# Kernel tuning notes

Hardware: AMD Instinct MI355X
Metric: run time of the kernel (lower is better)

## Reference

```python
import jax, jax.numpy as jnp
import numpy as np
import math

B, H, T, DH, D = 1, 8, 2048, 64, 64
NEG_INF = -1e30
EPS = 1e-9

def setup_inputs() -> dict:
    key = jax.random.key(0)
    ks = jax.random.split(key, 6)
    q = jax.random.normal(ks[0], (B, H, T, DH), dtype=jnp.float32)
    k = jax.random.normal(ks[1], (B, H, T, DH), dtype=jnp.float32)
    v = jax.random.normal(ks[2], (B, H, T, DH), dtype=jnp.float32)
    edge_type_bias = 0.1 * jax.random.normal(ks[3], (4,), dtype=jnp.float32)
    neigh_idx = jax.random.randint(ks[4], (H, T, D), 0, T).astype(jnp.int32)
    edge_type = jax.random.randint(ks[5], (H, T, D), 0, 5).astype(jnp.int32)
    return {"q": q, "k": k, "v": v, "edge_type_bias": edge_type_bias,
            "neigh_idx": neigh_idx, "edge_type": edge_type}

def _masked_softmax(scores, mask):
    # scores: [B,H,T,D] fp32, mask: [1,H,T,D] bool; zeros on all-masked rows
    masked = jnp.where(mask, scores, NEG_INF)
    m = jnp.max(masked, axis=-1, keepdims=True)
    e = jnp.where(mask, jnp.exp(masked - m), 0.0)
    denom = jnp.maximum(jnp.sum(e, axis=-1, keepdims=True), EPS)
    return e / denom

def reference(q, k, v, edge_type_bias, neigh_idx, edge_type):
    Bq, Hq, Tq, dh = q.shape
    # safe_neighbor_idx: clamp to valid range
    s_idx = jnp.clip(neigh_idx, 0, Tq - 1)                       # [H,T,D]
    # causal_neighbor_mask: valid (>=0) and neighbor <= query position
    pos = jnp.arange(Tq, dtype=neigh_idx.dtype)[None, :, None]    # [1,T,1]
    mask = (neigh_idx >= 0) & (neigh_idx <= pos)                  # [H,T,D]
    # edge-type bias: type 0 -> no bias, types 1..4 -> learnable bias
    full_bias = jnp.concatenate([jnp.zeros((1,), jnp.float32),
                                 edge_type_bias.astype(jnp.float32)])
    bias_htd = full_bias[edge_type]                               # [H,T,D]
    # gather neighbor K/V: k_g[b,h,t,n,:] = k[b,h,s_idx[h,t,n],:]
    h_ix = jnp.arange(Hq)[:, None, None]                          # [H,1,1]
    k_g = k[:, h_ix, s_idx]                                       # [B,H,T,D,dh]
    v_g = v[:, h_ix, s_idx]                                       # [B,H,T,D,dh]
    scores = jnp.einsum('bhtc,bhtnc->bhtn',
                        q.astype(jnp.float32),
                        k_g.astype(jnp.float32)) / math.sqrt(dh)
    scores = scores + bias_htd[None]                              # [B,H,T,D]
    w = _masked_softmax(scores, mask[None])                       # [B,H,T,D]
    y = jnp.einsum('bhtn,bhtnc->bhtc', w, v_g.astype(jnp.float32))
    return y.astype(v.dtype)
```

## Files before the change

### kernel.cpp

```cpp
#include <hip/hip_runtime.h>
#include <hip/hip_fp16.h>

constexpr int H  = 8;
constexpr int T  = 2048;
constexpr int DH = 64;
constexpr int D  = 64;
constexpr int NKV = H * T * DH;

typedef _Float16 half2v __attribute__((ext_vector_type(2)));

#if defined(__has_builtin)
#if __has_builtin(__builtin_amdgcn_fdot2)
#define HAVE_FDOT2 1
#endif
#if __has_builtin(__builtin_amdgcn_permlane32_swap)
#define HAVE_PL32 1
#endif
#if __has_builtin(__builtin_amdgcn_permlane16_swap)
#define HAVE_PL16 1
#endif
#endif

__device__ __forceinline__ float dot2acc(half2v a, half2v b, float c) {
#ifdef HAVE_FDOT2
    return __builtin_amdgcn_fdot2(a, b, c, false);
#else
    return c + (float)a.x * (float)b.x + (float)a.y * (float)b.y;
#endif
}

__device__ __forceinline__ half2v h2bits(int b) { return __builtin_bit_cast(half2v, b); }

__device__ __forceinline__ half2v f2h2(float x, float y) {
    __half2 h = __float22half2_rn(make_float2(x, y));
    return __builtin_bit_cast(half2v, h);
}

__device__ __forceinline__ float xor32add_f(float x) {
#ifdef HAVE_PL32
    unsigned u = __builtin_bit_cast(unsigned, x);
    auto r = __builtin_amdgcn_permlane32_swap(u, u, false, false);
    return __builtin_bit_cast(float, (unsigned)r[0]) + __builtin_bit_cast(float, (unsigned)r[1]);
#else
    return x + __shfl_xor(x, 32);
#endif
}
__device__ __forceinline__ float xor32max_f(float x) {
#ifdef HAVE_PL32
    unsigned u = __builtin_bit_cast(unsigned, x);
    auto r = __builtin_amdgcn_permlane32_swap(u, u, false, false);
    return fmaxf(__builtin_bit_cast(float, (unsigned)r[0]), __builtin_bit_cast(float, (unsigned)r[1]));
#else
    return fmaxf(x, __shfl_xor(x, 32));
#endif
}
__device__ __forceinline__ float xor16add_f(float x) {
#ifdef HAVE_PL16
    unsigned u = __builtin_bit_cast(unsigned, x);
    auto r = __builtin_amdgcn_permlane16_swap(u, u, false, false);
    return __builtin_bit_cast(float, (unsigned)r[0]) + __builtin_bit_cast(float, (unsigned)r[1]);
#else
    return x + __shfl_xor(x, 16);
#endif
}
__device__ __forceinline__ float xor16max_f(float x) {
#ifdef HAVE_PL16
    unsigned u = __builtin_bit_cast(unsigned, x);
    auto r = __builtin_amdgcn_permlane16_swap(u, u, false, false);
    return fmaxf(__builtin_bit_cast(float, (unsigned)r[0]), __builtin_bit_cast(float, (unsigned)r[1]));
#else
    return fmaxf(x, __shfl_xor(x, 16));
#endif
}
__device__ __forceinline__ half2v xor32add_h2(half2v x) {
#ifdef HAVE_PL32
    unsigned u = __builtin_bit_cast(unsigned, x);
    auto r = __builtin_amdgcn_permlane32_swap(u, u, false, false);
    return h2bits((int)r[0]) + h2bits((int)r[1]);
#else
    return x + h2bits(__shfl_xor(__builtin_bit_cast(int, x), 32));
#endif
}
__device__ __forceinline__ half2v xor16add_h2(half2v x) {
#ifdef HAVE_PL16
    unsigned u = __builtin_bit_cast(unsigned, x);
    auto r = __builtin_amdgcn_permlane16_swap(u, u, false, false);
    return h2bits((int)r[0]) + h2bits((int)r[1]);
#else
    return x + h2bits(__shfl_xor(__builtin_bit_cast(int, x), 16));
#endif
}
__device__ __forceinline__ half2v xor8add_h2(half2v x) {
    return x + h2bits(__shfl_xor(__builtin_bit_cast(int, x), 8));
}

__global__ __launch_bounds__(256) void cvt_f32_f16(
    const float* __restrict__ k, const float* __restrict__ v,
    __half* __restrict__ kh, __half* __restrict__ vh)
{
    const int i = (blockIdx.x * 256 + threadIdx.x) * 8;
    const float* src = (blockIdx.y == 0) ? k : v;
    __half*      dst = (blockIdx.y == 0) ? kh : vh;
    const float4 a = *reinterpret_cast<const float4*>(src + i);
    const float4 b = *reinterpret_cast<const float4*>(src + i + 4);
    __half2 hh[4];
    hh[0] = __float22half2_rn(make_float2(a.x, a.y));
    hh[1] = __float22half2_rn(make_float2(a.z, a.w));
    hh[2] = __float22half2_rn(make_float2(b.x, b.y));
    hh[3] = __float22half2_rn(make_float2(b.z, b.w));
    *reinterpret_cast<float4*>(dst + i) = *reinterpret_cast<const float4*>(hh);
}

__global__ __launch_bounds__(256, 5) void wayfinder_attn_f16(
    const float* __restrict__ q,
    const __half* __restrict__ kh,
    const __half* __restrict__ vh,
    const float* __restrict__ eb,
    const int*   __restrict__ nidx,
    const int*   __restrict__ etyp,
    float* __restrict__ out)
{
    __shared__ __half vlds[4][8][512];

    const int wave = threadIdx.x >> 6;
    const int lane = threadIdx.x & 63;
    const int bid  = blockIdx.x;
    const int work = ((bid & 7) << 9) | (bid >> 3);
    const int flat = (work << 2) + wave;
    const int h    = flat >> 11;
    const int t    = flat & (T - 1);
    const int grp  = lane >> 3;
    const int sub  = lane & 7;

    const long long rowoff = (long long)flat * DH;
    const int*      nrow   = nidx + (long long)flat * D;
    const int*      erow   = etyp + (long long)flat * D;

    const int4 i0 = *reinterpret_cast<const int4*>(nrow + grp * 8);
    const int4 i1 = *reinterpret_cast<const int4*>(nrow + grp * 8 + 4);
    const int4 e0 = *reinterpret_cast<const int4*>(erow + grp * 8);
    const int4 e1 = *reinterpret_cast<const int4*>(erow + grp * 8 + 4);

    const float4 qa = *reinterpret_cast<const float4*>(q + rowoff + sub * 8);
    const float4 qb = *reinterpret_cast<const float4*>(q + rowoff + sub * 8 + 4);

    const int idx_i[8] = {i0.x, i0.y, i0.z, i0.w, i1.x, i1.y, i1.z, i1.w};
    const int et_i [8] = {e0.x, e0.y, e0.z, e0.w, e1.x, e1.y, e1.z, e1.w};

    const __half* khead = kh + (long long)h * T * DH;
    const __half* vhead = vh + (long long)h * T * DH;

    int s_i[8];
    int mskbits = 0;
    #pragma unroll
    for (int i = 0; i < 8; ++i) {
        s_i[i] = min(max(idx_i[i], 0), T - 1);
        mskbits |= ((idx_i[i] >= 0) && (idx_i[i] <= t)) ? (1 << i) : 0;
    }

    float4 kf[8];
    #pragma unroll
    for (int i = 0; i < 8; ++i)
        kf[i] = *reinterpret_cast<const float4*>(khead + (long long)s_i[i] * DH + sub * 8);

    #pragma unroll
    for (int i = 0; i < 8; ++i) {
        const __half* src = vhead + (long long)s_i[i] * DH + sub * 8;
        __builtin_amdgcn_global_load_lds(
            (const __attribute__((address_space(1))) void*)src,
            (__attribute__((address_space(3))) void*)(&vlds[wave][i][0]),
            16, 0, 0);
    }

    const float4 ebv = *reinterpret_cast<const float4*>(eb);
    float bias_i[8];
    #pragma unroll
    for (int i = 0; i < 8; ++i) {
        const int et = et_i[i];
        bias_i[i] = (et == 1) ? ebv.x : (et == 2) ? ebv.y :
                    (et == 3) ? ebv.z : (et == 4) ? ebv.w : 0.0f;
    }

    half2v qp[4];
    qp[0] = f2h2(qa.x, qa.y);
    qp[1] = f2h2(qa.z, qa.w);
    qp[2] = f2h2(qb.x, qb.y);
    qp[3] = f2h2(qb.z, qb.w);

    float sc[8];
    #pragma unroll
    for (int i = 0; i < 8; ++i) {
        const half2v* kp = reinterpret_cast<const half2v*>(&kf[i]);
        float p = dot2acc(qp[0], kp[0],
                  dot2acc(qp[1], kp[1],
                  dot2acc(qp[2], kp[2],
                  dot2acc(qp[3], kp[3], 0.0f))));
        p += __shfl_xor(p, 1);
        p += __shfl_xor(p, 2);
        p += __shfl_xor(p, 4);
        sc[i] = p;
    }

    float masked[8];
    float mx = -1e30f;
    #pragma unroll
    for (int i = 0; i < 8; ++i) {
        const bool mk = (mskbits >> i) & 1;
        masked[i] = mk ? fmaf(sc[i], 0.125f, bias_i[i]) : -1e30f;
        mx = fmaxf(mx, masked[i]);
    }
    mx = fmaxf(mx, __shfl_xor(mx, 8));
    mx = xor16max_f(mx);
    mx = xor32max_f(mx);

    float e[8];
    float sum = 0.0f;
    #pragma unroll
    for (int i = 0; i < 8; ++i) {
        const bool mk = (mskbits >> i) & 1;
        e[i] = mk ? __expf(masked[i] - mx) : 0.0f;
        sum += e[i];
    }
    sum += __shfl_xor(sum, 8);
    sum = xor16add_f(sum);
    sum = xor32add_f(sum);
    const float rden = 1.0f / fmaxf(sum, 1e-9f);

    asm volatile("s_waitcnt vmcnt(0)" ::: "memory");

    float acc[8] = {0.f, 0.f, 0.f, 0.f, 0.f, 0.f, 0.f, 0.f};
    #pragma unroll
    for (int i = 0; i < 8; ++i) {
        const float w = e[i] * rden;
        const float4 vfi = *reinterpret_cast<const float4*>(&vlds[wave][i][lane * 8]);
        const half2v* vp = reinterpret_cast<const half2v*>(&vfi);
        acc[0] += w * (float)vp[0].x;  acc[1] += w * (float)vp[0].y;
        acc[2] += w * (float)vp[1].x;  acc[3] += w * (float)vp[1].y;
        acc[4] += w * (float)vp[2].x;  acc[5] += w * (float)vp[2].y;
        acc[6] += w * (float)vp[3].x;  acc[7] += w * (float)vp[3].y;
    }

    half2v h0 = f2h2(acc[0], acc[1]);
    half2v h1 = f2h2(acc[2], acc[3]);
    half2v h2 = f2h2(acc[4], acc[5]);
    half2v h3 = f2h2(acc[6], acc[7]);
    h0 = xor8add_h2(h0);  h1 = xor8add_h2(h1);
    h2 = xor8add_h2(h2);  h3 = xor8add_h2(h3);
    h0 = xor16add_h2(h0); h1 = xor16add_h2(h1);
    h2 = xor16add_h2(h2); h3 = xor16add_h2(h3);
    h0 = xor32add_h2(h0); h1 = xor32add_h2(h1);
    h2 = xor32add_h2(h2); h3 = xor32add_h2(h3);

    if (lane < 16) {
        const int s8   = (lane & 7) * 8;
        const int half = lane >> 3;
        const float4 o = half
            ? make_float4((float)h2.x, (float)h2.y, (float)h3.x, (float)h3.y)
            : make_float4((float)h0.x, (float)h0.y, (float)h1.x, (float)h1.y);
        *reinterpret_cast<float4*>(out + rowoff + s8 + half * 4) = o;
    }
}

__global__ __launch_bounds__(256) void wayfinder_attn_f32(
    const float* __restrict__ q, const float* __restrict__ k,
    const float* __restrict__ v, const float* __restrict__ eb,
    const int* __restrict__ nidx, const int* __restrict__ etyp,
    float* __restrict__ out)
{
    const int wave = threadIdx.x >> 6;
    const int lane = threadIdx.x & 63;
    const int flat = (blockIdx.x << 2) + wave;
    const int h    = flat >> 11;
    const int t    = flat & (T - 1);
    const int grp  = lane >> 4;
    const int sub  = lane & 15;

    __shared__ int    sidx[4][64];
    __shared__ float  ssc [4][64];
    __shared__ float2 swv [4][64];

    const long long rowoff = (long long)flat * DH;
    const long long noff = (long long)flat * D + lane;
    const int  idx = nidx[noff];
    const int  et  = etyp[noff];
    const int  s   = min(max(idx, 0), T - 1);
    const bool msk = (idx >= 0) && (idx <= t);
    const float4 ebv  = *reinterpret_cast<const float4*>(eb);
    const float  bias = (et == 1) ? ebv.x : (et == 2) ? ebv.y :
                        (et == 3) ? ebv.z : (et == 4) ? ebv.w : 0.0f;
    sidx[wave][lane] = s;
    const float4 qf = *reinterpret_cast<const float4*>(q + rowoff + sub * 4);
    __syncthreads();

    const float* khead = k + (long long)h * T * DH;
    #pragma unroll
    for (int i = 0; i < 16; ++i) {
        const int n  = i * 4 + grp;
        const int sn = sidx[wave][n];
        const float4 kf = *reinterpret_cast<const float4*>(khead + sn * DH + sub * 4);
        float p = qf.x * kf.x + qf.y * kf.y + qf.z * kf.z + qf.w * kf.w;
        p += __shfl_xor(p, 1);
        p += __shfl_xor(p, 2);
        p += __shfl_xor(p, 4);
        p += __shfl_xor(p, 8);
        if (sub == 0) ssc[wave][n] = p;
    }
    __syncthreads();

    const float sc     = ssc[wave][lane];
    const float masked = msk ? (sc * 0.125f + bias) : -1e30f;
    float mx = masked;
    #pragma unroll
    for (int off = 32; off > 0; off >>= 1) mx = fmaxf(mx, __shfl_xor(mx, off));
    const float e = msk ? __expf(masked - mx) : 0.0f;
    float sum = e;
    #pragma unroll
    for (int off = 32; off > 0; off >>= 1) sum += __shfl_xor(sum, off);
    const float w = e / fmaxf(sum, 1e-9f);
    swv[wave][lane] = make_float2(w, __int_as_float(s));
    __syncthreads();

    const float* vhead = v + (long long)h * T * DH;
    float4 acc = make_float4(0.f, 0.f, 0.f, 0.f);
    #pragma unroll
    for (int i = 0; i < 16; ++i) {
        const int    n  = i * 4 + grp;
        const float2 ws = swv[wave][n];
        const int    sn = __float_as_int(ws.y);
        const float4 vf = *reinterpret_cast<const float4*>(vhead + sn * DH + sub * 4);
        acc.x += ws.x * vf.x; acc.y += ws.x * vf.y;
        acc.z += ws.x * vf.z; acc.w += ws.x * vf.w;
    }
    #pragma unroll
    for (int off = 16; off <= 32; off <<= 1) {
        acc.x += __shfl_xor(acc.x, off); acc.y += __shfl_xor(acc.y, off);
        acc.z += __shfl_xor(acc.z, off); acc.w += __shfl_xor(acc.w, off);
    }
    if (lane < 16)
        *reinterpret_cast<float4*>(out + rowoff + sub * 4) = acc;
}

extern "C" void kernel_launch(void* const* d_in, const int* in_sizes, int n_in,
                              void* d_out, int out_size, void* d_ws, size_t ws_size,
                              hipStream_t stream) {
    const float* q    = (const float*)d_in[0];
    const float* k    = (const float*)d_in[1];
    const float* v    = (const float*)d_in[2];
    const float* eb   = (const float*)d_in[3];
    const int*   nidx = (const int*)d_in[4];
    const int*   etyp = (const int*)d_in[5];
    float* out = (float*)d_out;

    const size_t need = (size_t)2 * NKV * sizeof(__half);
    if (ws_size >= need) {
        __half* kh = (__half*)d_ws;
        __half* vh = kh + NKV;
        dim3 cgrid(NKV / (256 * 8), 2);
        hipLaunchKernelGGL(cvt_f32_f16, cgrid, dim3(256), 0, stream, k, v, kh, vh);
        hipLaunchKernelGGL(wayfinder_attn_f16, dim3(H * T / 4), dim3(256), 0, stream,
                           q, kh, vh, eb, nidx, etyp, out);
    } else {
        hipLaunchKernelGGL(wayfinder_attn_f32, dim3(H * T / 4), dim3(256), 0, stream,
                           q, k, v, eb, nidx, etyp, out);
    }
}
```

Before: 29.55 us.

## Load gathered V rows into registers and use DPP for lane reductions

Gathered V rows are now loaded directly into registers next to the K loads, replacing the asynchronous global-to-LDS copy. This removes the shared-memory buffer and the explicit vmcnt wait. The xor-1/2/4/8 shuffle reductions become DPP quad-permute and row-mirror moves, which avoid the cross-lane shuffle path. The min-occupancy hint in launch_bounds is dropped, so the compiler can use more registers for the extra 8 float4 V values, which may reduce occupancy and latency hiding.

```diff
diff --git a/kernel.cpp b/kernel.cpp
--- a/kernel.cpp
+++ b/kernel.cpp
@@ -35,6 +35,17 @@
     __half2 h = __float22half2_rn(make_float2(x, y));
     return __builtin_bit_cast(half2v, h);
 }
+
+template<int CTRL>
+__device__ __forceinline__ float dpp_mov_f(float x) {
+    int yi = __builtin_amdgcn_update_dpp(0, __builtin_bit_cast(int, x),
+                                         CTRL, 0xF, 0xF, true);
+    return __builtin_bit_cast(float, yi);
+}
+template<int CTRL>
+__device__ __forceinline__ float dpp_add_f(float x) { return x + dpp_mov_f<CTRL>(x); }
+template<int CTRL>
+__device__ __forceinline__ float dpp_max_f(float x) { return fmaxf(x, dpp_mov_f<CTRL>(x)); }
 
 __device__ __forceinline__ float xor32add_f(float x) {
 #ifdef HAVE_PL32
@@ -111,7 +122,7 @@
     *reinterpret_cast<float4*>(dst + i) = *reinterpret_cast<const float4*>(hh);
 }
 
-__global__ __launch_bounds__(256, 5) void wayfinder_attn_f16(
+__global__ __launch_bounds__(256) void wayfinder_attn_f16(
     const float* __restrict__ q,
     const __half* __restrict__ kh,
     const __half* __restrict__ vh,
@@ -120,8 +131,6 @@
     const int*   __restrict__ etyp,
     float* __restrict__ out)
 {
-    __shared__ __half vlds[4][8][512];
-
     const int wave = threadIdx.x >> 6;
     const int lane = threadIdx.x & 63;
     const int bid  = blockIdx.x;
@@ -158,18 +167,12 @@
         mskbits |= ((idx_i[i] >= 0) && (idx_i[i] <= t)) ? (1 << i) : 0;
     }
 
-    float4 kf[8];
-    #pragma unroll
-    for (int i = 0; i < 8; ++i)
-        kf[i] = *reinterpret_cast<const float4*>(khead + (long long)s_i[i] * DH + sub * 8);
-
-    #pragma unroll
-    for (int i = 0; i < 8; ++i) {
-        const __half* src = vhead + (long long)s_i[i] * DH + sub * 8;
-        __builtin_amdgcn_global_load_lds(
-            (const __attribute__((address_space(1))) void*)src,
-            (__attribute__((address_space(3))) void*)(&vlds[wave][i][0]),
-            16, 0, 0);
+    float4 kf[8], vf[8];
+    #pragma unroll
+    for (int i = 0; i < 8; ++i) {
+        const long long ro = (long long)s_i[i] * DH + sub * 8;
+        kf[i] = *reinterpret_cast<const float4*>(khead + ro);
+        vf[i] = *reinterpret_cast<const float4*>(vhead + ro);
     }
 
     const float4 ebv = *reinterpret_cast<const float4*>(eb);
@@ -195,9 +198,9 @@
                   dot2acc(qp[1], kp[1],
                   dot2acc(qp[2], kp[2],
                   dot2acc(qp[3], kp[3], 0.0f))));
-        p += __shfl_xor(p, 1);
-        p += __shfl_xor(p, 2);
-        p += __shfl_xor(p, 4);
+        p = dpp_add_f<0xB1>(p);
+        p = dpp_add_f<0x4E>(p);
+        p = dpp_add_f<0x141>(p);
         sc[i] = p;
     }
 
@@ -209,7 +212,7 @@
         masked[i] = mk ? fmaf(sc[i], 0.125f, bias_i[i]) : -1e30f;
         mx = fmaxf(mx, masked[i]);
     }
-    mx = fmaxf(mx, __shfl_xor(mx, 8));
+    mx = dpp_max_f<0x140>(mx);
     mx = xor16max_f(mx);
     mx = xor32max_f(mx);
 
@@ -221,19 +224,16 @@
         e[i] = mk ? __expf(masked[i] - mx) : 0.0f;
         sum += e[i];
     }
-    sum += __shfl_xor(sum, 8);
+    sum = dpp_add_f<0x140>(sum);
     sum = xor16add_f(sum);
     sum = xor32add_f(sum);
     const float rden = 1.0f / fmaxf(sum, 1e-9f);
 
-    asm volatile("s_waitcnt vmcnt(0)" ::: "memory");
-
     float acc[8] = {0.f, 0.f, 0.f, 0.f, 0.f, 0.f, 0.f, 0.f};
     #pragma unroll
     for (int i = 0; i < 8; ++i) {
         const float w = e[i] * rden;
-        const float4 vfi = *reinterpret_cast<const float4*>(&vlds[wave][i][lane * 8]);
-        const half2v* vp = reinterpret_cast<const half2v*>(&vfi);
+        const half2v* vp = reinterpret_cast<const half2v*>(&vf[i]);
         acc[0] += w * (float)vp[0].x;  acc[1] += w * (float)vp[0].y;
         acc[2] += w * (float)vp[1].x;  acc[3] += w * (float)vp[1].y;
         acc[4] += w * (float)vp[2].x;  acc[5] += w * (float)vp[2].y;
```

New measurement: 25.32 us (median of 2 runs). 14.3% less time.
